# Kernel optimization log

Measured on AMD Instinct MI355X. Metric: run time of the kernel, lower is better.

## Reference

```python
import jax, jax.numpy as jnp
import numpy as np
import math

D_MODEL = 512
N_HEADS = 2
B, S = 2, 1024
THRESHOLD = 0.5  # kwargs default 'sparsity_threshold'


def setup_inputs() -> dict:
    key = jax.random.key(0)
    ks = jax.random.split(key, 10)
    D, H = D_MODEL, D_MODEL // 4
    std = 0.02
    return {
        "x": jax.random.normal(ks[0], (B, S, D), jnp.float32),
        "Wq": jax.random.normal(ks[1], (D, D), jnp.float32) * std,
        "Wk": jax.random.normal(ks[2], (D, D), jnp.float32) * std,
        "Wv": jax.random.normal(ks[3], (D, D), jnp.float32) * std,
        "Wo": jax.random.normal(ks[4], (D, D), jnp.float32) * std,
        "bo": jnp.zeros((D,), jnp.float32),
        "W1": jax.random.normal(ks[5], (D, H), jnp.float32) * std,
        "b1": jnp.zeros((H,), jnp.float32),
        "W2": jax.random.normal(ks[6], (H, 1), jnp.float32) * std,
        "b2": jnp.zeros((1,), jnp.float32),
    }


def reference(x, Wq, Wk, Wv, Wo, bo, W1, b1, W2, b2):
    Bsz, Seq, D = x.shape
    Hn = N_HEADS
    dh = D // Hn

    def split_heads(t):
        return t.reshape(Bsz, Seq, Hn, dh).transpose(0, 2, 1, 3)  # [B,H,S,dh]

    q = split_heads(x @ Wq)
    k = split_heads(x @ Wk)
    v = split_heads(x @ Wv)

    scores = jnp.einsum("bhid,bhjd->bhij", q, k) / math.sqrt(dh)  # [B,H,S,S]

    # head-mean features for the pairwise sparsity predictor (n_heads==2 => 2*dh == D)
    q_mean = q.mean(axis=1)  # [B,S,dh]
    k_mean = k.mean(axis=1)  # [B,S,dh]
    # Linear1 of cat([q_mean_i, k_mean_j]) splits into two halves of W1
    a = q_mean @ W1[:dh]   # [B,S,Dh4]
    c = k_mean @ W1[dh:]   # [B,S,Dh4]
    hidden = jax.nn.relu(a[:, :, None, :] + c[:, None, :, :] + b1)  # [B,S,S,Dh4]
    connection_probs = jax.nn.sigmoid(jnp.squeeze(hidden @ W2, -1) + b2[0])  # [B,S,S]

    mask = connection_probs > THRESHOLD  # [B,S,S]
    scores = jnp.where(mask[:, None, :, :], scores, jnp.float32(-1e9))
    attn = jax.nn.softmax(scores, axis=-1)  # dropout inactive in eval

    out = jnp.einsum("bhij,bhjd->bhid", attn, v)  # [B,H,S,dh]
    out = out.transpose(0, 2, 1, 3).reshape(Bsz, Seq, D)
    out = out @ Wo + bo
    return out
```

## Files before the change

kernel.cpp:

```cpp
#include <hip/hip_runtime.h>


typedef unsigned short u16t;
typedef __bf16 bf16x8 __attribute__((ext_vector_type(8)));
typedef float f32x4 __attribute__((ext_vector_type(4)));

#define B_SZ 2
#define S_SZ 1024
#define D_SZ 512
#define DH 256
#define HH 128

static __device__ __forceinline__ u16t f2b(float f) {
    unsigned int u = __builtin_bit_cast(unsigned int, f);
    u += 0x7FFFu + ((u >> 16) & 1u);
    return (u16t)(u >> 16);
}

static __device__ __forceinline__ f32x4 mfma16(bf16x8 a, bf16x8 b, f32x4 c) {
    return __builtin_amdgcn_mfma_f32_16x16x32_bf16(a, b, c, 0, 0, 0);
}

static __device__ __forceinline__ void gload16(const void* g, void* l) {
    __builtin_amdgcn_global_load_lds(
        (const __attribute__((address_space(1))) void*)g,
        (__attribute__((address_space(3))) void*)l, 16, 0, 0);
}

__global__ __launch_bounds__(256) void k_prep(
    const float* __restrict__ x,
    const float* __restrict__ Wq, const float* __restrict__ Wk,
    const float* __restrict__ Wv, const float* __restrict__ Wo,
    const float* __restrict__ W1,
    u16t* __restrict__ xb, u16t* __restrict__ WT, float* __restrict__ Beff)
{
    __shared__ float smf[1088];
    int bidx = blockIdx.x;
    int t = threadIdx.x;
    if (bidx < 1024) {
        int idx = (bidx * 256 + t) * 4;
        float4 v = *(const float4*)(x + idx);
        u16t* o = xb + idx;
        o[0] = f2b(v.x); o[1] = f2b(v.y); o[2] = f2b(v.z); o[3] = f2b(v.w);
    } else if (bidx < 2048) {
        int t2 = bidx - 1024;
        int z = t2 >> 8, rem = t2 & 255;
        int n0 = (rem & 15) * 32, k0 = (rem >> 4) * 32;
        const float* W = z == 0 ? Wq : z == 1 ? Wk : z == 2 ? Wv : Wo;
        u16t* WTz = WT + (size_t)z * D_SZ * D_SZ;
        float (*tile)[33] = (float(*)[33])smf;
        int r = t >> 3, c4 = (t & 7) * 4;
        float4 v = *(const float4*)(W + (size_t)(k0 + r) * D_SZ + n0 + c4);
        tile[r][c4] = v.x; tile[r][c4 + 1] = v.y; tile[r][c4 + 2] = v.z; tile[r][c4 + 3] = v.w;
        __syncthreads();
        u16t o[4];
        o[0] = f2b(tile[c4][r]); o[1] = f2b(tile[c4 + 1][r]);
        o[2] = f2b(tile[c4 + 2][r]); o[3] = f2b(tile[c4 + 3][r]);
        *(ushort4*)(WTz + (size_t)(n0 + r) * D_SZ + k0 + c4) = *(ushort4*)o;
    } else {
        int k = bidx - 2048;
        float* wm0 = smf;
        float* wm1 = smf + 256;
        const float* wrq = Wq + (size_t)k * D_SZ;
        const float* wrk = Wk + (size_t)k * D_SZ;
        wm0[t & 255] = 0.5f * (wrq[t & 255] + wrq[(t & 255) + DH]);
        wm1[t & 255] = 0.5f * (wrk[t & 255] + wrk[(t & 255) + DH]);
        __syncthreads();
        int half = t >> 7, hcol = t & 127;
        const float* wm = half ? wm1 : wm0;
        const float* W1h = W1 + (half ? (size_t)DH * HH : 0);
        float s = 0.f;
        for (int d = 0; d < 256; ++d) s += wm[d] * W1h[(size_t)d * HH + hcol];
        Beff[(size_t)k * 256 + half * 128 + hcol] = s;
    }
}

template<int MF, int NF>
static __device__ __forceinline__ void gemm_db(
    const u16t* __restrict__ A, int lda, const u16t* __restrict__ B, int ldb,
    int K, int tid, u16t* Als, u16t* Bls, f32x4 acc[MF][NF])
{
    const int w = tid >> 6, lane = tid & 63;
    const int lr = lane & 15, kg = lane >> 4;
    const int srow = lane >> 3;
    const int scol = ((lane & 7) ^ srow) * 8;
    const int ABUF = MF * 4096;
    const int BBUF = NF * 1024;
    auto stage = [&](int bb, int k0) {
#pragma unroll
        for (int q = 0; q < MF * 2; ++q) {
            int ci = w * (MF * 2) + q;
            gload16(A + (size_t)(ci * 8 + srow) * lda + k0 + scol,
                    Als + bb * ABUF + ci * 512);
        }
#pragma unroll
        for (int q = 0; q < NF / 2; ++q) {
            int cj = w * (NF / 2) + q;
            gload16(B + (size_t)(cj * 8 + srow) * ldb + k0 + scol,
                    Bls + bb * BBUF + cj * 512);
        }
    };
    stage(0, 0);
    __syncthreads();
    const int nt = K / 64;
    for (int t = 0; t < nt; ++t) {
        int cur = t & 1;
        if (t + 1 < nt) stage(cur ^ 1, (t + 1) * 64);
        const u16t* Ab = Als + cur * ABUF;
        const u16t* Bb = Bls + cur * BBUF;
#pragma unroll
        for (int kk = 0; kk < 2; ++kk) {
            bf16x8 af[MF], bfr[NF];
#pragma unroll
            for (int fi = 0; fi < MF; ++fi) {
                int r = w * (MF * 16) + fi * 16 + lr;
                af[fi] = *(const bf16x8*)(&Ab[r * 64 + (((kk * 4 + kg) ^ (r & 7)) << 3)]);
            }
#pragma unroll
            for (int fj = 0; fj < NF; ++fj) {
                int r = fj * 16 + lr;
                bfr[fj] = *(const bf16x8*)(&Bb[r * 64 + (((kk * 4 + kg) ^ (r & 7)) << 3)]);
            }
#pragma unroll
            for (int fi = 0; fi < MF; ++fi)
#pragma unroll
                for (int fj = 0; fj < NF; ++fj)
                    acc[fi][fj] = mfma16(af[fi], bfr[fj], acc[fi][fj]);
        }
        __syncthreads();
    }
}


__global__ __launch_bounds__(256) void k_qkvac(
    const u16t* __restrict__ xb, const u16t* __restrict__ WT,
    const float* __restrict__ x, const float* __restrict__ Beff,
    const float* __restrict__ b1,
    u16t* __restrict__ qb, u16t* __restrict__ kb, u16t* __restrict__ vT,
    float* __restrict__ a, float* __restrict__ cc)
{
    __shared__ __align__(16) char sm[49152];
    int bid = blockIdx.x;
    int t = threadIdx.x;
    if (bid < 384) {
        u16t* Als = (u16t*)sm;
        u16t* Bls = (u16t*)(sm + 32768);
        int z = bid / 128, rem = bid & 127;
        int m0 = (rem >> 3) * 128, n0 = (rem & 7) * 64;
        const u16t* A = xb + (size_t)m0 * D_SZ;
        const u16t* Bt = WT + (size_t)z * D_SZ * D_SZ + (size_t)n0 * D_SZ;
        f32x4 acc[2][4] = {};
        gemm_db<2, 4>(A, D_SZ, Bt, D_SZ, D_SZ, t, Als, Bls, acc);
        int w = t >> 6, lane = t & 63, lr = lane & 15, kg = lane >> 4;
        if (z < 2) {
            u16t (*vls)[68] = (u16t(*)[68])sm;
            float scale = z == 0 ? 0.0625f : 1.0f;
#pragma unroll
            for (int fi = 0; fi < 2; ++fi)
#pragma unroll
                for (int fj = 0; fj < 4; ++fj)
#pragma unroll
                    for (int rr = 0; rr < 4; ++rr)
                        vls[w * 32 + fi * 16 + kg * 4 + rr][fj * 16 + lr]
                            = f2b(acc[fi][fj][rr] * scale);
            __syncthreads();
            u16t* dst = z == 0 ? qb : kb;
            int c8 = (t & 7) * 8, r0 = t >> 3;
#pragma unroll
            for (int p = 0; p < 4; ++p) {
                int r = r0 + p * 32;
                *(uint4*)(dst + (size_t)(m0 + r) * D_SZ + n0 + c8) = *(const uint4*)(&vls[r][c8]);
            }
        } else {
            u16t (*vls)[136] = (u16t(*)[136])sm;
#pragma unroll
            for (int fi = 0; fi < 2; ++fi)
#pragma unroll
                for (int fj = 0; fj < 4; ++fj)
#pragma unroll
                    for (int rr = 0; rr < 4; ++rr)
                        vls[fj * 16 + lr][w * 32 + fi * 16 + kg * 4 + rr] = f2b(acc[fi][fj][rr]);
            __syncthreads();
            int b = m0 >> 10, s0 = m0 & 1023;
            int cr = t >> 2, seg = t & 3;
            const u16t* srcp = &vls[cr][seg * 32];
            u16t* dstp = vT + (((size_t)(b * D_SZ + n0 + cr)) << 10) + s0 + seg * 32;
#pragma unroll
            for (int qq = 0; qq < 4; ++qq)
                *(uint4*)(dstp + qq * 8) = *(const uint4*)(srcp + qq * 8);
        }
    } else {
        float (*xs)[68] = (float(*)[68])sm;
        float (*bsT)[68] = (float(*)[68])(sm + 17408);
        int t2 = bid - 384;
        int r0 = (t2 & 31) * 64, n0 = (t2 >> 5) * 32;
        int ti = t >> 4, tj = t & 15;
        float acc[4][2] = {};
        for (int k0 = 0; k0 < 512; k0 += 64) {
            if (k0) __syncthreads();
#pragma unroll
            for (int p = 0; p < 4; ++p) {
                int idx = t + p * 256;
                int r = idx >> 4, c4 = (idx & 15) * 4;
                *(float4*)&xs[r][c4] = *(const float4*)(x + (size_t)(r0 + r) * D_SZ + k0 + c4);
            }
#pragma unroll
            for (int p = 0; p < 2; ++p) {
                int idx = t + p * 256;
                int k = idx >> 3, n4 = (idx & 7) * 4;
                float4 v = *(const float4*)(Beff + (size_t)(k0 + k) * 256 + n0 + n4);
                bsT[n4][k] = v.x; bsT[n4 + 1][k] = v.y; bsT[n4 + 2][k] = v.z; bsT[n4 + 3][k] = v.w;
            }
            __syncthreads();
#pragma unroll
            for (int kk = 0; kk < 16; ++kk) {
                float4 xv[4], bv[2];
#pragma unroll
                for (int ri = 0; ri < 4; ++ri) xv[ri] = *(const float4*)&xs[ti + 16 * ri][kk * 4];
#pragma unroll
                for (int rj = 0; rj < 2; ++rj) bv[rj] = *(const float4*)&bsT[tj + 16 * rj][kk * 4];
#pragma unroll
                for (int ri = 0; ri < 4; ++ri)
#pragma unroll
                    for (int rj = 0; rj < 2; ++rj)
                        acc[ri][rj] += xv[ri].x * bv[rj].x + xv[ri].y * bv[rj].y
                                     + xv[ri].z * bv[rj].z + xv[ri].w * bv[rj].w;
            }
        }
        bool isA = n0 < 128;
#pragma unroll
        for (int rj = 0; rj < 2; ++rj) {
            int col = n0 + tj + 16 * rj;
            float badd = isA ? b1[col] : 0.f;
#pragma unroll
            for (int ri = 0; ri < 4; ++ri) {
                int row = r0 + ti + 16 * ri;
                if (isA) a[(size_t)row * HH + col] = acc[ri][rj] + badd;
                else     cc[(size_t)row * HH + (col - 128)] = acc[ri][rj];
            }
        }
    }
}

__global__ __launch_bounds__(256) void k_scores(
    const u16t* __restrict__ qb, const u16t* __restrict__ kb,
    const float* __restrict__ a, const float* __restrict__ c,
    const float* __restrict__ W2, const float* __restrict__ b2,
    u16t* __restrict__ P, float* __restrict__ lpart)
{
    __shared__ __align__(16) char sm[36864];
    float (*at)[132] = (float(*)[132])sm;
    float (*ct)[132] = (float(*)[132])(sm + 16896);
    unsigned char (*msk)[64] = (unsigned char(*)[64])(sm + 33792);
    float* w2s  = (float*)(sm + 35840);
    float* lsum = (float*)(sm + 36352);
    int b = blockIdx.z, mt = blockIdx.y, jb = blockIdx.x;
    int m0 = mt * 32, j0 = jb * 64;
    int t = threadIdx.x;
    if (t < 128) w2s[t] = W2[t];
    float fb2 = b2[0];
    int ti = t >> 4, tj = t & 15;
#pragma unroll
    for (int p = 0; p < 4; ++p) {
        int idx = t + p * 256;
        int r = idx >> 5, c4 = (idx & 31) * 4;
        *(float4*)&at[r][c4] = *(const float4*)(a + ((size_t)(b * S_SZ + m0 + r)) * HH + c4);
    }
#pragma unroll
    for (int jh = 0; jh < 2; ++jh) {
        __syncthreads();
#pragma unroll
        for (int p = 0; p < 4; ++p) {
            int idx = t + p * 256;
            int r = idx >> 5, c4 = (idx & 31) * 4;
            *(float4*)&ct[r][c4] =
                *(const float4*)(c + ((size_t)(b * S_SZ + j0 + jh * 32 + r)) * HH + c4);
        }
        __syncthreads();
        float accm[2][2];
#pragma unroll
        for (int ri = 0; ri < 2; ++ri)
#pragma unroll
            for (int rj = 0; rj < 2; ++rj) accm[ri][rj] = fb2;
#pragma unroll 2
        for (int h4 = 0; h4 < 32; ++h4) {
            float4 wv = ((const float4*)w2s)[h4];
            float4 av[2], cv[2];
#pragma unroll
            for (int ri = 0; ri < 2; ++ri) av[ri] = *(const float4*)&at[ti + 16 * ri][h4 * 4];
#pragma unroll
            for (int rj = 0; rj < 2; ++rj) cv[rj] = *(const float4*)&ct[tj + 16 * rj][h4 * 4];
#pragma unroll
            for (int ri = 0; ri < 2; ++ri)
#pragma unroll
                for (int rj = 0; rj < 2; ++rj) {
                    accm[ri][rj] += fmaxf(av[ri].x + cv[rj].x, 0.f) * wv.x;
                    accm[ri][rj] += fmaxf(av[ri].y + cv[rj].y, 0.f) * wv.y;
                    accm[ri][rj] += fmaxf(av[ri].z + cv[rj].z, 0.f) * wv.z;
                    accm[ri][rj] += fmaxf(av[ri].w + cv[rj].w, 0.f) * wv.w;
                }
        }
#pragma unroll
        for (int ri = 0; ri < 2; ++ri)
#pragma unroll
            for (int rj = 0; rj < 2; ++rj)
                msk[ti + 16 * ri][jh * 32 + tj + 16 * rj] = accm[ri][rj] > 0.f ? 1 : 0;
    }
    __syncthreads();
    u16t* Als = (u16t*)sm;
    u16t* Bls = (u16t*)(sm + 8192);
    const u16t* A = qb + (size_t)(b * S_SZ + m0) * D_SZ;
    const u16t* B = kb + (size_t)(b * S_SZ + j0) * D_SZ;
    const int w = t >> 6, lane = t & 63, lr = lane & 15, kg = lane >> 4;
    const int srow = lane >> 3;
    const int scol = ((lane & 7) ^ srow) * 8;
    auto stage = [&](int bb, int k0) {
        gload16(A + (size_t)(w * 8 + srow) * D_SZ + k0 + scol, Als + bb * 2048 + w * 512);
#pragma unroll
        for (int q = 0; q < 2; ++q) {
            int cj = w * 2 + q;
            gload16(B + (size_t)(cj * 8 + srow) * D_SZ + k0 + scol, Bls + bb * 4096 + cj * 512);
        }
    };
    f32x4 acc0[2] = {}, acc1[2] = {};
    stage(0, 0);
    __syncthreads();
#pragma unroll
    for (int t8 = 0; t8 < 8; ++t8) {
        int cur = t8 & 1;
        if (t8 < 7) stage(cur ^ 1, (t8 + 1) * 64);
        const u16t* Ab = Als + cur * 2048;
        const u16t* Bb = Bls + cur * 4096;
#pragma unroll
        for (int kk = 0; kk < 2; ++kk) {
            int rb = w * 16 + lr;
            bf16x8 bfr = *(const bf16x8*)(&Bb[rb * 64 + (((kk * 4 + kg) ^ (rb & 7)) << 3)]);
            bf16x8 af[2];
#pragma unroll
            for (int fi = 0; fi < 2; ++fi) {
                int ra = fi * 16 + lr;
                af[fi] = *(const bf16x8*)(&Ab[ra * 64 + (((kk * 4 + kg) ^ (ra & 7)) << 3)]);
            }
            if (t8 < 4) {
#pragma unroll
                for (int fi = 0; fi < 2; ++fi) acc0[fi] = mfma16(af[fi], bfr, acc0[fi]);
            } else {
#pragma unroll
                for (int fi = 0; fi < 2; ++fi) acc1[fi] = mfma16(af[fi], bfr, acc1[fi]);
            }
        }
        __syncthreads();
    }
    u16t (*vls)[68] = (u16t(*)[68])sm;
#pragma unroll
    for (int h = 0; h < 2; ++h) {
#pragma unroll
        for (int fi = 0; fi < 2; ++fi)
#pragma unroll
            for (int rr = 0; rr < 4; ++rr) {
                int il = fi * 16 + kg * 4 + rr;
                int jl = w * 16 + lr;
                float s = h ? acc1[fi][rr] : acc0[fi][rr];
                float e = msk[il][jl] ? __expf(s) : 0.f;
                if (h) acc1[fi][rr] = e; else acc0[fi][rr] = e;
            }
#pragma unroll
        for (int fi = 0; fi < 2; ++fi)
#pragma unroll
            for (int rr = 0; rr < 4; ++rr) {
                float rs = h ? acc1[fi][rr] : acc0[fi][rr];
                rs += __shfl_xor(rs, 1); rs += __shfl_xor(rs, 2);
                rs += __shfl_xor(rs, 4); rs += __shfl_xor(rs, 8);
                if (lr == 0) lsum[w * 32 + fi * 16 + kg * 4 + rr] = rs;
            }
        __syncthreads();
        if (t < 32) {
            float l = lsum[t] + lsum[32 + t] + lsum[64 + t] + lsum[96 + t];
            lpart[((size_t)(jb * 4 + b * 2 + h) << 10) + m0 + t] = l;
        }
#pragma unroll
        for (int fi = 0; fi < 2; ++fi)
#pragma unroll
            for (int rr = 0; rr < 4; ++rr)
                vls[fi * 16 + kg * 4 + rr][w * 16 + lr]
                    = f2b(h ? acc1[fi][rr] : acc0[fi][rr]);
        __syncthreads();
        int r = t >> 3, c8 = (t & 7) * 8;
        *(uint4*)(P + ((size_t)(b * 2 + h) << 20) + ((size_t)(m0 + r) << 10) + j0 + c8)
            = *(const uint4*)(&vls[r][c8]);
        __syncthreads();
    }
}

__global__ __launch_bounds__(256) void k_pv(
    const u16t* __restrict__ P, const u16t* __restrict__ vT,
    const float* __restrict__ lpart, u16t* __restrict__ ao)
{
    __shared__ __align__(16) u16t sm[12288];
    __shared__ float invl[64];
    u16t* Als = sm;
    u16t* Bls = sm + 8192;
    int bh = blockIdx.z, b = bh >> 1, h = bh & 1;
    int m0 = blockIdx.y * 64, n0 = blockIdx.x * 32;
    int t = threadIdx.x;
    if (t < 64) {
        float l = 0.f;
        for (int jb = 0; jb < 16; ++jb)
            l += lpart[((size_t)(jb * 4 + bh) << 10) + m0 + t];
        invl[t] = l > 0.f ? 1.0f / l : 0.f;
    }
    const u16t* A = P + ((size_t)bh << 20) + (size_t)m0 * S_SZ;
    const u16t* Bt = vT + ((size_t)(b * D_SZ + h * DH + n0)) * S_SZ;
    f32x4 acc[1][2] = {};
    gemm_db<1, 2>(A, S_SZ, Bt, S_SZ, S_SZ, t, Als, Bls, acc);
    int w = t >> 6, lane = t & 63, lr = lane & 15, kg = lane >> 4;
    u16t (*ols)[40] = (u16t(*)[40])sm;
#pragma unroll
    for (int fj = 0; fj < 2; ++fj)
#pragma unroll
        for (int rr = 0; rr < 4; ++rr) {
            int rl = w * 16 + kg * 4 + rr;
            ols[rl][fj * 16 + lr] = f2b(acc[0][fj][rr] * invl[rl]);
        }
    __syncthreads();
    int r = t >> 2, c8 = (t & 3) * 8;
    *(uint4*)(ao + ((size_t)(b * S_SZ + m0 + r)) * D_SZ + h * DH + n0 + c8)
        = *(const uint4*)(&ols[r][c8]);
}

__global__ __launch_bounds__(256) void k_out(
    const u16t* __restrict__ ao, const u16t* __restrict__ WoT,
    const float* __restrict__ bo, float* __restrict__ out)
{
    __shared__ __align__(16) u16t sm[12288];
    u16t* Als = sm;
    u16t* Bls = sm + 8192;
    int m0 = blockIdx.y * 64, n0 = blockIdx.x * 32;
    const u16t* A = ao + (size_t)m0 * D_SZ;
    const u16t* Bt = WoT + (size_t)n0 * D_SZ;
    f32x4 acc[1][2] = {};
    gemm_db<1, 2>(A, D_SZ, Bt, D_SZ, D_SZ, threadIdx.x, Als, Bls, acc);
    int w = threadIdx.x >> 6, lane = threadIdx.x & 63, lr = lane & 15, kg = lane >> 4;
    float (*ols)[36] = (float(*)[36])sm;
#pragma unroll
    for (int fj = 0; fj < 2; ++fj)
#pragma unroll
        for (int rr = 0; rr < 4; ++rr) {
            int rl = w * 16 + kg * 4 + rr;
            ols[rl][fj * 16 + lr] = acc[0][fj][rr] + bo[n0 + fj * 16 + lr];
        }
    __syncthreads();
    int r0 = threadIdx.x >> 3, c4 = (threadIdx.x & 7) * 4;
#pragma unroll
    for (int p = 0; p < 2; ++p) {
        int r = r0 + p * 32;
        *(float4*)(out + (size_t)(m0 + r) * D_SZ + n0 + c4) = *(const float4*)(&ols[r][c4]);
    }
}

extern "C" void kernel_launch(void* const* d_in, const int* in_sizes, int n_in,
                              void* d_out, int out_size, void* d_ws, size_t ws_size,
                              hipStream_t stream)
{
    const float* x  = (const float*)d_in[0];
    const float* Wq = (const float*)d_in[1];
    const float* Wk = (const float*)d_in[2];
    const float* Wv = (const float*)d_in[3];
    const float* Wo = (const float*)d_in[4];
    const float* bo = (const float*)d_in[5];
    const float* W1 = (const float*)d_in[6];
    const float* b1 = (const float*)d_in[7];
    const float* W2 = (const float*)d_in[8];
    const float* b2 = (const float*)d_in[9];
    float* out = (float*)d_out;

    char* ws = (char*)d_ws;
    size_t off = 0;
    auto carve = [&](size_t bytes) { void* p = ws + off; off += (bytes + 255) & ~(size_t)255; return p; };
    u16t* xb   = (u16t*)carve((size_t)2048 * 512 * 2);
    u16t* WT   = (u16t*)carve((size_t)4 * 512 * 512 * 2);
    u16t* qb   = (u16t*)carve((size_t)2048 * 512 * 2);
    u16t* kb   = (u16t*)carve((size_t)2048 * 512 * 2);
    u16t* vT   = (u16t*)carve((size_t)2 * 512 * 1024 * 2);
    float* Beff = (float*)carve((size_t)512 * 256 * 4);
    float* a   = (float*)carve((size_t)2048 * 128 * 4);
    float* c   = (float*)carve((size_t)2048 * 128 * 4);
    u16t* P    = (u16t*)carve((size_t)4 * 1024 * 1024 * 2);
    float* lpart = (float*)carve((size_t)16 * 4 * 1024 * 4);
    u16t* ao   = (u16t*)carve((size_t)2048 * 512 * 2);
    (void)ws_size;

    k_prep<<<dim3(2560), dim3(256), 0, stream>>>(x, Wq, Wk, Wv, Wo, W1, xb, WT, Beff);
    k_qkvac<<<dim3(640), dim3(256), 0, stream>>>(xb, WT, x, Beff, b1, qb, kb, vT, a, c);
    k_scores<<<dim3(16, 32, 2), dim3(256), 0, stream>>>(qb, kb, a, c, W2, b2, P, lpart);
    k_pv<<<dim3(8, 16, 4), dim3(256), 0, stream>>>(P, vT, lpart, ao);
    k_out<<<dim3(16, 32), dim3(256), 0, stream>>>(ao, WT + (size_t)3 * 512 * 512, bo, out);
}
```

Before: 99.78 us.

## Fuse five kernels into one cooperative persistent megakernel with grid syncs

Replaces the five separate kernel launches with a single cooperative kernel of 512 blocks that loops over the virtual blocks of each phase and separates phases with grid-wide syncs. To fit 32KB shared memory at two blocks per CU, the QKV GEMM tile shrinks from 128 to 64 rows and the mask MLP computes one key column per thread instead of two. The goal is to remove launch gaps and inter-kernel tail effects. The costs are grid-sync overhead, a per-call host occupancy and device-property query, and lower per-block reuse from the smaller tiles. A fallback runs the phases as separate kernels if the cooperative launch is unavailable.

```diff
diff --git a/kernel.cpp b/kernel.cpp
--- a/kernel.cpp
+++ b/kernel.cpp
@@ -1,5 +1,8 @@
 #include <hip/hip_runtime.h>
-
+#include <hip/hip_cooperative_groups.h>
+
+
+namespace cg = cooperative_groups;
 
 typedef unsigned short u16t;
 typedef __bf16 bf16x8 __attribute__((ext_vector_type(8)));
@@ -25,54 +28,6 @@
     __builtin_amdgcn_global_load_lds(
         (const __attribute__((address_space(1))) void*)g,
         (__attribute__((address_space(3))) void*)l, 16, 0, 0);
-}
-
-__global__ __launch_bounds__(256) void k_prep(
-    const float* __restrict__ x,
-    const float* __restrict__ Wq, const float* __restrict__ Wk,
-    const float* __restrict__ Wv, const float* __restrict__ Wo,
-    const float* __restrict__ W1,
-    u16t* __restrict__ xb, u16t* __restrict__ WT, float* __restrict__ Beff)
-{
-    __shared__ float smf[1088];
-    int bidx = blockIdx.x;
-    int t = threadIdx.x;
-    if (bidx < 1024) {
-        int idx = (bidx * 256 + t) * 4;
-        float4 v = *(const float4*)(x + idx);
-        u16t* o = xb + idx;
-        o[0] = f2b(v.x); o[1] = f2b(v.y); o[2] = f2b(v.z); o[3] = f2b(v.w);
-    } else if (bidx < 2048) {
-        int t2 = bidx - 1024;
-        int z = t2 >> 8, rem = t2 & 255;
-        int n0 = (rem & 15) * 32, k0 = (rem >> 4) * 32;
-        const float* W = z == 0 ? Wq : z == 1 ? Wk : z == 2 ? Wv : Wo;
-        u16t* WTz = WT + (size_t)z * D_SZ * D_SZ;
-        float (*tile)[33] = (float(*)[33])smf;
-        int r = t >> 3, c4 = (t & 7) * 4;
-        float4 v = *(const float4*)(W + (size_t)(k0 + r) * D_SZ + n0 + c4);
-        tile[r][c4] = v.x; tile[r][c4 + 1] = v.y; tile[r][c4 + 2] = v.z; tile[r][c4 + 3] = v.w;
-        __syncthreads();
-        u16t o[4];
-        o[0] = f2b(tile[c4][r]); o[1] = f2b(tile[c4 + 1][r]);
-        o[2] = f2b(tile[c4 + 2][r]); o[3] = f2b(tile[c4 + 3][r]);
-        *(ushort4*)(WTz + (size_t)(n0 + r) * D_SZ + k0 + c4) = *(ushort4*)o;
-    } else {
-        int k = bidx - 2048;
-        float* wm0 = smf;
-        float* wm1 = smf + 256;
-        const float* wrq = Wq + (size_t)k * D_SZ;
-        const float* wrk = Wk + (size_t)k * D_SZ;
-        wm0[t & 255] = 0.5f * (wrq[t & 255] + wrq[(t & 255) + DH]);
-        wm1[t & 255] = 0.5f * (wrk[t & 255] + wrk[(t & 255) + DH]);
-        __syncthreads();
-        int half = t >> 7, hcol = t & 127;
-        const float* wm = half ? wm1 : wm0;
-        const float* W1h = W1 + (half ? (size_t)DH * HH : 0);
-        float s = 0.f;
-        for (int d = 0; d < 256; ++d) s += wm[d] * W1h[(size_t)d * HH + hcol];
-        Beff[(size_t)k * 256 + half * 128 + hcol] = s;
-    }
 }
 
 template<int MF, int NF>
@@ -132,67 +87,101 @@
 }
 
 
-__global__ __launch_bounds__(256) void k_qkvac(
-    const u16t* __restrict__ xb, const u16t* __restrict__ WT,
-    const float* __restrict__ x, const float* __restrict__ Beff,
-    const float* __restrict__ b1,
-    u16t* __restrict__ qb, u16t* __restrict__ kb, u16t* __restrict__ vT,
-    float* __restrict__ a, float* __restrict__ cc)
-{
-    __shared__ __align__(16) char sm[49152];
-    int bid = blockIdx.x;
-    int t = threadIdx.x;
-    if (bid < 384) {
+static __device__ void ph_prep(int vb, int t, char* sm,
+    const float* x, const float* Wq, const float* Wk, const float* Wv,
+    const float* Wo, const float* W1,
+    u16t* xb, u16t* WT, float* Beff)
+{
+    float* smf = (float*)sm;
+    if (vb < 1024) {
+        int idx = (vb * 256 + t) * 4;
+        float4 v = *(const float4*)(x + idx);
+        u16t* o = xb + idx;
+        o[0] = f2b(v.x); o[1] = f2b(v.y); o[2] = f2b(v.z); o[3] = f2b(v.w);
+    } else if (vb < 2048) {
+        int t2 = vb - 1024;
+        int z = t2 >> 8, rem = t2 & 255;
+        int n0 = (rem & 15) * 32, k0 = (rem >> 4) * 32;
+        const float* W = z == 0 ? Wq : z == 1 ? Wk : z == 2 ? Wv : Wo;
+        u16t* WTz = WT + (size_t)z * D_SZ * D_SZ;
+        float (*tile)[33] = (float(*)[33])smf;
+        int r = t >> 3, c4 = (t & 7) * 4;
+        float4 v = *(const float4*)(W + (size_t)(k0 + r) * D_SZ + n0 + c4);
+        tile[r][c4] = v.x; tile[r][c4 + 1] = v.y; tile[r][c4 + 2] = v.z; tile[r][c4 + 3] = v.w;
+        __syncthreads();
+        u16t o[4];
+        o[0] = f2b(tile[c4][r]); o[1] = f2b(tile[c4 + 1][r]);
+        o[2] = f2b(tile[c4 + 2][r]); o[3] = f2b(tile[c4 + 3][r]);
+        *(ushort4*)(WTz + (size_t)(n0 + r) * D_SZ + k0 + c4) = *(ushort4*)o;
+    } else {
+        int k = vb - 2048;
+        float* wm0 = smf;
+        float* wm1 = smf + 256;
+        const float* wrq = Wq + (size_t)k * D_SZ;
+        const float* wrk = Wk + (size_t)k * D_SZ;
+        wm0[t & 255] = 0.5f * (wrq[t & 255] + wrq[(t & 255) + DH]);
+        wm1[t & 255] = 0.5f * (wrk[t & 255] + wrk[(t & 255) + DH]);
+        __syncthreads();
+        int half = t >> 7, hcol = t & 127;
+        const float* wm = half ? wm1 : wm0;
+        const float* W1h = W1 + (half ? (size_t)DH * HH : 0);
+        float s = 0.f;
+        for (int d = 0; d < 256; ++d) s += wm[d] * W1h[(size_t)d * HH + hcol];
+        Beff[(size_t)k * 256 + half * 128 + hcol] = s;
+    }
+}
+
+static __device__ void ph_qkvac(int vb, int t, char* sm,
+    const u16t* xb, const u16t* WT, const float* x, const float* Beff,
+    const float* b1,
+    u16t* qb, u16t* kb, u16t* vT, float* a, float* cc)
+{
+    if (vb < 768) {
         u16t* Als = (u16t*)sm;
-        u16t* Bls = (u16t*)(sm + 32768);
-        int z = bid / 128, rem = bid & 127;
-        int m0 = (rem >> 3) * 128, n0 = (rem & 7) * 64;
+        u16t* Bls = (u16t*)(sm + 16384);
+        int z = vb >> 8, rem = vb & 255;
+        int m0 = (rem >> 3) * 64, n0 = (rem & 7) * 64;
         const u16t* A = xb + (size_t)m0 * D_SZ;
         const u16t* Bt = WT + (size_t)z * D_SZ * D_SZ + (size_t)n0 * D_SZ;
-        f32x4 acc[2][4] = {};
-        gemm_db<2, 4>(A, D_SZ, Bt, D_SZ, D_SZ, t, Als, Bls, acc);
+        f32x4 acc[1][4] = {};
+        gemm_db<1, 4>(A, D_SZ, Bt, D_SZ, D_SZ, t, Als, Bls, acc);
         int w = t >> 6, lane = t & 63, lr = lane & 15, kg = lane >> 4;
         if (z < 2) {
             u16t (*vls)[68] = (u16t(*)[68])sm;
             float scale = z == 0 ? 0.0625f : 1.0f;
 #pragma unroll
-            for (int fi = 0; fi < 2; ++fi)
-#pragma unroll
-                for (int fj = 0; fj < 4; ++fj)
-#pragma unroll
-                    for (int rr = 0; rr < 4; ++rr)
-                        vls[w * 32 + fi * 16 + kg * 4 + rr][fj * 16 + lr]
-                            = f2b(acc[fi][fj][rr] * scale);
+            for (int fj = 0; fj < 4; ++fj)
+#pragma unroll
+                for (int rr = 0; rr < 4; ++rr)
+                    vls[w * 16 + kg * 4 + rr][fj * 16 + lr]
+                        = f2b(acc[0][fj][rr] * scale);
             __syncthreads();
             u16t* dst = z == 0 ? qb : kb;
             int c8 = (t & 7) * 8, r0 = t >> 3;
 #pragma unroll
-            for (int p = 0; p < 4; ++p) {
+            for (int p = 0; p < 2; ++p) {
                 int r = r0 + p * 32;
                 *(uint4*)(dst + (size_t)(m0 + r) * D_SZ + n0 + c8) = *(const uint4*)(&vls[r][c8]);
             }
         } else {
-            u16t (*vls)[136] = (u16t(*)[136])sm;
-#pragma unroll
-            for (int fi = 0; fi < 2; ++fi)
-#pragma unroll
-                for (int fj = 0; fj < 4; ++fj)
-#pragma unroll
-                    for (int rr = 0; rr < 4; ++rr)
-                        vls[fj * 16 + lr][w * 32 + fi * 16 + kg * 4 + rr] = f2b(acc[fi][fj][rr]);
+            u16t (*vls)[72] = (u16t(*)[72])sm;
+#pragma unroll
+            for (int fj = 0; fj < 4; ++fj)
+#pragma unroll
+                for (int rr = 0; rr < 4; ++rr)
+                    vls[fj * 16 + lr][w * 16 + kg * 4 + rr] = f2b(acc[0][fj][rr]);
             __syncthreads();
             int b = m0 >> 10, s0 = m0 & 1023;
             int cr = t >> 2, seg = t & 3;
-            const u16t* srcp = &vls[cr][seg * 32];
-            u16t* dstp = vT + (((size_t)(b * D_SZ + n0 + cr)) << 10) + s0 + seg * 32;
-#pragma unroll
-            for (int qq = 0; qq < 4; ++qq)
-                *(uint4*)(dstp + qq * 8) = *(const uint4*)(srcp + qq * 8);
+            const u16t* srcp = &vls[cr][seg * 16];
+            u16t* dstp = vT + (((size_t)(b * D_SZ + n0 + cr)) << 10) + s0 + seg * 16;
+            *(uint4*)dstp = *(const uint4*)srcp;
+            *(uint4*)(dstp + 8) = *(const uint4*)(srcp + 8);
         }
     } else {
         float (*xs)[68] = (float(*)[68])sm;
         float (*bsT)[68] = (float(*)[68])(sm + 17408);
-        int t2 = bid - 384;
+        int t2 = vb - 768;
         int r0 = (t2 & 31) * 64, n0 = (t2 >> 5) * 32;
         int ti = t >> 4, tj = t & 15;
         float acc[4][2] = {};
@@ -242,21 +231,17 @@
     }
 }
 
-__global__ __launch_bounds__(256) void k_scores(
-    const u16t* __restrict__ qb, const u16t* __restrict__ kb,
-    const float* __restrict__ a, const float* __restrict__ c,
-    const float* __restrict__ W2, const float* __restrict__ b2,
-    u16t* __restrict__ P, float* __restrict__ lpart)
-{
-    __shared__ __align__(16) char sm[36864];
+static __device__ void ph_scores(int vb, int t, char* sm,
+    const u16t* qb, const u16t* kb, const float* a, const float* cc,
+    const float* W2, const float* b2, u16t* P, float* lpart)
+{
     float (*at)[132] = (float(*)[132])sm;
     float (*ct)[132] = (float(*)[132])(sm + 16896);
-    unsigned char (*msk)[64] = (unsigned char(*)[64])(sm + 33792);
-    float* w2s  = (float*)(sm + 35840);
-    float* lsum = (float*)(sm + 36352);
-    int b = blockIdx.z, mt = blockIdx.y, jb = blockIdx.x;
+    unsigned char (*msk)[64] = (unsigned char(*)[64])(sm + 26624);
+    float* w2s  = (float*)(sm + 28672);
+    float* lsum = (float*)(sm + 29184);
+    int jb = vb & 15, mt = (vb >> 4) & 31, b = vb >> 9;
     int m0 = mt * 32, j0 = jb * 64;
-    int t = threadIdx.x;
     if (t < 128) w2s[t] = W2[t];
     float fb2 = b2[0];
     int ti = t >> 4, tj = t & 15;
@@ -267,44 +252,34 @@
         *(float4*)&at[r][c4] = *(const float4*)(a + ((size_t)(b * S_SZ + m0 + r)) * HH + c4);
     }
 #pragma unroll
-    for (int jh = 0; jh < 2; ++jh) {
-        __syncthreads();
-#pragma unroll
-        for (int p = 0; p < 4; ++p) {
+    for (int jq = 0; jq < 4; ++jq) {
+        __syncthreads();
+#pragma unroll
+        for (int p = 0; p < 2; ++p) {
             int idx = t + p * 256;
             int r = idx >> 5, c4 = (idx & 31) * 4;
             *(float4*)&ct[r][c4] =
-                *(const float4*)(c + ((size_t)(b * S_SZ + j0 + jh * 32 + r)) * HH + c4);
-        }
-        __syncthreads();
-        float accm[2][2];
-#pragma unroll
-        for (int ri = 0; ri < 2; ++ri)
-#pragma unroll
-            for (int rj = 0; rj < 2; ++rj) accm[ri][rj] = fb2;
+                *(const float4*)(cc + ((size_t)(b * S_SZ + j0 + jq * 16 + r)) * HH + c4);
+        }
+        __syncthreads();
+        float accm[2];
+        accm[0] = fb2; accm[1] = fb2;
 #pragma unroll 2
         for (int h4 = 0; h4 < 32; ++h4) {
             float4 wv = ((const float4*)w2s)[h4];
-            float4 av[2], cv[2];
-#pragma unroll
-            for (int ri = 0; ri < 2; ++ri) av[ri] = *(const float4*)&at[ti + 16 * ri][h4 * 4];
-#pragma unroll
-            for (int rj = 0; rj < 2; ++rj) cv[rj] = *(const float4*)&ct[tj + 16 * rj][h4 * 4];
-#pragma unroll
-            for (int ri = 0; ri < 2; ++ri)
-#pragma unroll
-                for (int rj = 0; rj < 2; ++rj) {
-                    accm[ri][rj] += fmaxf(av[ri].x + cv[rj].x, 0.f) * wv.x;
-                    accm[ri][rj] += fmaxf(av[ri].y + cv[rj].y, 0.f) * wv.y;
-                    accm[ri][rj] += fmaxf(av[ri].z + cv[rj].z, 0.f) * wv.z;
-                    accm[ri][rj] += fmaxf(av[ri].w + cv[rj].w, 0.f) * wv.w;
-                }
+            float4 cv = *(const float4*)&ct[tj][h4 * 4];
+#pragma unroll
+            for (int ri = 0; ri < 2; ++ri) {
+                float4 av = *(const float4*)&at[ti + 16 * ri][h4 * 4];
+                accm[ri] += fmaxf(av.x + cv.x, 0.f) * wv.x;
+                accm[ri] += fmaxf(av.y + cv.y, 0.f) * wv.y;
+                accm[ri] += fmaxf(av.z + cv.z, 0.f) * wv.z;
+                accm[ri] += fmaxf(av.w + cv.w, 0.f) * wv.w;
+            }
         }
 #pragma unroll
         for (int ri = 0; ri < 2; ++ri)
-#pragma unroll
-            for (int rj = 0; rj < 2; ++rj)
-                msk[ti + 16 * ri][jh * 32 + tj + 16 * rj] = accm[ri][rj] > 0.f ? 1 : 0;
+            msk[ti + 16 * ri][jq * 16 + tj] = accm[ri] > 0.f ? 1 : 0;
     }
     __syncthreads();
     u16t* Als = (u16t*)sm;
@@ -392,17 +367,15 @@
     }
 }
 
-__global__ __launch_bounds__(256) void k_pv(
-    const u16t* __restrict__ P, const u16t* __restrict__ vT,
-    const float* __restrict__ lpart, u16t* __restrict__ ao)
-{
-    __shared__ __align__(16) u16t sm[12288];
-    __shared__ float invl[64];
-    u16t* Als = sm;
-    u16t* Bls = sm + 8192;
-    int bh = blockIdx.z, b = bh >> 1, h = bh & 1;
-    int m0 = blockIdx.y * 64, n0 = blockIdx.x * 32;
-    int t = threadIdx.x;
+static __device__ void ph_pv(int vb, int t, char* sm,
+    const u16t* P, const u16t* vT, const float* lpart, u16t* ao)
+{
+    u16t* Als = (u16t*)sm;
+    u16t* Bls = (u16t*)(sm + 16384);
+    float* invl = (float*)(sm + 24576);
+    int xw = vb & 7, yw = (vb >> 3) & 15, bh = vb >> 7;
+    int b = bh >> 1, h = bh & 1;
+    int m0 = yw * 64, n0 = xw * 32;
     if (t < 64) {
         float l = 0.f;
         for (int jb = 0; jb < 16; ++jb)
@@ -428,19 +401,17 @@
         = *(const uint4*)(&ols[r][c8]);
 }
 
-__global__ __launch_bounds__(256) void k_out(
-    const u16t* __restrict__ ao, const u16t* __restrict__ WoT,
-    const float* __restrict__ bo, float* __restrict__ out)
-{
-    __shared__ __align__(16) u16t sm[12288];
-    u16t* Als = sm;
-    u16t* Bls = sm + 8192;
-    int m0 = blockIdx.y * 64, n0 = blockIdx.x * 32;
+static __device__ void ph_out(int vb, int t, char* sm,
+    const u16t* ao, const u16t* WT, const float* bo, float* out)
+{
+    u16t* Als = (u16t*)sm;
+    u16t* Bls = (u16t*)(sm + 16384);
+    int m0 = (vb >> 4) * 64, n0 = (vb & 15) * 32;
     const u16t* A = ao + (size_t)m0 * D_SZ;
-    const u16t* Bt = WoT + (size_t)n0 * D_SZ;
+    const u16t* Bt = WT + (size_t)3 * D_SZ * D_SZ + (size_t)n0 * D_SZ;
     f32x4 acc[1][2] = {};
-    gemm_db<1, 2>(A, D_SZ, Bt, D_SZ, D_SZ, threadIdx.x, Als, Bls, acc);
-    int w = threadIdx.x >> 6, lane = threadIdx.x & 63, lr = lane & 15, kg = lane >> 4;
+    gemm_db<1, 2>(A, D_SZ, Bt, D_SZ, D_SZ, t, Als, Bls, acc);
+    int w = t >> 6, lane = t & 63, lr = lane & 15, kg = lane >> 4;
     float (*ols)[36] = (float(*)[36])sm;
 #pragma unroll
     for (int fj = 0; fj < 2; ++fj)
@@ -450,12 +421,90 @@
             ols[rl][fj * 16 + lr] = acc[0][fj][rr] + bo[n0 + fj * 16 + lr];
         }
     __syncthreads();
-    int r0 = threadIdx.x >> 3, c4 = (threadIdx.x & 7) * 4;
+    int r0 = t >> 3, c4 = (t & 7) * 4;
 #pragma unroll
     for (int p = 0; p < 2; ++p) {
         int r = r0 + p * 32;
         *(float4*)(out + (size_t)(m0 + r) * D_SZ + n0 + c4) = *(const float4*)(&ols[r][c4]);
     }
+}
+
+
+__global__ __launch_bounds__(256, 2) void k_mega(
+    const float* __restrict__ x,
+    const float* __restrict__ Wq, const float* __restrict__ Wk,
+    const float* __restrict__ Wv, const float* __restrict__ Wo,
+    const float* __restrict__ bo, const float* __restrict__ W1,
+    const float* __restrict__ b1, const float* __restrict__ W2,
+    const float* __restrict__ b2,
+    u16t* __restrict__ xb, u16t* __restrict__ WT, float* __restrict__ Beff,
+    u16t* __restrict__ qb, u16t* __restrict__ kb, u16t* __restrict__ vT,
+    float* __restrict__ a, float* __restrict__ cc,
+    u16t* __restrict__ P, float* __restrict__ lpart,
+    u16t* __restrict__ ao, float* __restrict__ out)
+{
+    __shared__ __align__(16) char sm[32768];
+    cg::grid_group grid = cg::this_grid();
+    const int G = gridDim.x;
+    const int t = threadIdx.x;
+    for (int vb = blockIdx.x; vb < 2560; vb += G) {
+        ph_prep(vb, t, sm, x, Wq, Wk, Wv, Wo, W1, xb, WT, Beff);
+        __syncthreads();
+    }
+    grid.sync();
+    for (int vb = blockIdx.x; vb < 1024; vb += G) {
+        ph_qkvac(vb, t, sm, xb, WT, x, Beff, b1, qb, kb, vT, a, cc);
+        __syncthreads();
+    }
+    grid.sync();
+    for (int vb = blockIdx.x; vb < 1024; vb += G) {
+        ph_scores(vb, t, sm, qb, kb, a, cc, W2, b2, P, lpart);
+        __syncthreads();
+    }
+    grid.sync();
+    for (int vb = blockIdx.x; vb < 512; vb += G) {
+        ph_pv(vb, t, sm, P, vT, lpart, ao);
+        __syncthreads();
+    }
+    grid.sync();
+    for (int vb = blockIdx.x; vb < 512; vb += G) {
+        ph_out(vb, t, sm, ao, WT, bo, out);
+        __syncthreads();
+    }
+}
+
+__global__ __launch_bounds__(256) void kw_prep(
+    const float* x, const float* Wq, const float* Wk, const float* Wv,
+    const float* Wo, const float* W1, u16t* xb, u16t* WT, float* Beff)
+{
+    __shared__ __align__(16) char sm[32768];
+    ph_prep(blockIdx.x, threadIdx.x, sm, x, Wq, Wk, Wv, Wo, W1, xb, WT, Beff);
+}
+__global__ __launch_bounds__(256) void kw_qkvac(
+    const u16t* xb, const u16t* WT, const float* x, const float* Beff,
+    const float* b1, u16t* qb, u16t* kb, u16t* vT, float* a, float* cc)
+{
+    __shared__ __align__(16) char sm[32768];
+    ph_qkvac(blockIdx.x, threadIdx.x, sm, xb, WT, x, Beff, b1, qb, kb, vT, a, cc);
+}
+__global__ __launch_bounds__(256) void kw_scores(
+    const u16t* qb, const u16t* kb, const float* a, const float* cc,
+    const float* W2, const float* b2, u16t* P, float* lpart)
+{
+    __shared__ __align__(16) char sm[32768];
+    ph_scores(blockIdx.x, threadIdx.x, sm, qb, kb, a, cc, W2, b2, P, lpart);
+}
+__global__ __launch_bounds__(256) void kw_pv(
+    const u16t* P, const u16t* vT, const float* lpart, u16t* ao)
+{
+    __shared__ __align__(16) char sm[32768];
+    ph_pv(blockIdx.x, threadIdx.x, sm, P, vT, lpart, ao);
+}
+__global__ __launch_bounds__(256) void kw_out(
+    const u16t* ao, const u16t* WT, const float* bo, float* out)
+{
+    __shared__ __align__(16) char sm[32768];
+    ph_out(blockIdx.x, threadIdx.x, sm, ao, WT, bo, out);
 }
 
 extern "C" void kernel_launch(void* const* d_in, const int* in_sizes, int n_in,
@@ -490,9 +539,35 @@
     u16t* ao   = (u16t*)carve((size_t)2048 * 512 * 2);
     (void)ws_size;
 
-    k_prep<<<dim3(2560), dim3(256), 0, stream>>>(x, Wq, Wk, Wv, Wo, W1, xb, WT, Beff);
-    k_qkvac<<<dim3(640), dim3(256), 0, stream>>>(xb, WT, x, Beff, b1, qb, kb, vT, a, c);
-    k_scores<<<dim3(16, 32, 2), dim3(256), 0, stream>>>(qb, kb, a, c, W2, b2, P, lpart);
-    k_pv<<<dim3(8, 16, 4), dim3(256), 0, stream>>>(P, vT, lpart, ao);
-    k_out<<<dim3(16, 32), dim3(256), 0, stream>>>(ao, WT + (size_t)3 * 512 * 512, bo, out);
-}
+    int nb = 0;
+    hipError_t qerr = hipOccupancyMaxActiveBlocksPerMultiprocessor(
+        &nb, (const void*)k_mega, 256, 0);
+    int numCU = 0;
+    {
+        hipDeviceProp_t prop;
+        int dev = 0;
+        if (hipGetDevice(&dev) == hipSuccess &&
+            hipGetDeviceProperties(&prop, dev) == hipSuccess)
+            numCU = prop.multiProcessorCount;
+    }
+    bool coop_ok = (qerr == hipSuccess) && (nb >= 1) && (numCU > 0) &&
+                   ((long)nb * numCU >= 512);
+    if (coop_ok) {
+        void* args[] = {
+            (void*)&x, (void*)&Wq, (void*)&Wk, (void*)&Wv, (void*)&Wo,
+            (void*)&bo, (void*)&W1, (void*)&b1, (void*)&W2, (void*)&b2,
+            (void*)&xb, (void*)&WT, (void*)&Beff, (void*)&qb, (void*)&kb,
+            (void*)&vT, (void*)&a, (void*)&c, (void*)&P, (void*)&lpart,
+            (void*)&ao, (void*)&out
+        };
+        hipError_t lerr = hipLaunchCooperativeKernel(
+            (const void*)k_mega, dim3(512), dim3(256), args, 0, stream);
+        if (lerr == hipSuccess) return;
+        (void)hipGetLastError();
+    }
+    kw_prep<<<dim3(2560), dim3(256), 0, stream>>>(x, Wq, Wk, Wv, Wo, W1, xb, WT, Beff);
+    kw_qkvac<<<dim3(1024), dim3(256), 0, stream>>>(xb, WT, x, Beff, b1, qb, kb, vT, a, c);
+    kw_scores<<<dim3(1024), dim3(256), 0, stream>>>(qb, kb, a, c, W2, b2, P, lpart);
+    kw_pv<<<dim3(512), dim3(256), 0, stream>>>(P, vT, lpart, ao);
+    kw_out<<<dim3(512), dim3(256), 0, stream>>>(ao, WT, bo, out);
+}
```

Result: slower. 148.3 us (+48.6%).
